# Performance work log

Hardware: AMD Instinct MI355X
Metric: run time of the kernel (lower is better)

## Reference

```python
import jax, jax.numpy as jnp
from jax import lax
import numpy as np

B, T, F = 128, 512, 64
U1_UNITS, U2_UNITS = 256, 128
W_SCALE = 0.05  # keep relu-activated cell state numerically stable


def lstm_relu(x, W, U, b, return_sequences):
    """Keras LSTM with activation='relu', recurrent_activation='sigmoid'.
    x: [B, T, D], W: [D, 4u], U: [u, 4u], b: [4u]. Gate order i, f, g, o.
    Dropout is inactive at inference and omitted."""
    Bsz = x.shape[0]
    units = U.shape[0]

    def step(carry, xt):
        h, c = carry
        z = xt @ W + h @ U + b  # [B, 4u]
        i, f, g, o = jnp.split(z, 4, axis=-1)
        i = jax.nn.sigmoid(i)
        f = jax.nn.sigmoid(f)
        g = jax.nn.relu(g)
        o = jax.nn.sigmoid(o)
        c_new = f * c + i * g
        h_new = o * jax.nn.relu(c_new)
        return (h_new, c_new), h_new

    xs = jnp.swapaxes(x, 0, 1)  # [T, B, D]
    init = (jnp.zeros((Bsz, units), x.dtype), jnp.zeros((Bsz, units), x.dtype))
    (h_last, _), hs = lax.scan(step, init, xs)
    if return_sequences:
        return jnp.swapaxes(hs, 0, 1)  # [B, T, u]
    return h_last  # [B, u]


def setup_inputs() -> dict:
    key = jax.random.key(0)
    ks = jax.random.split(key, 7)
    x = jax.random.normal(ks[0], (B, T, F), dtype=jnp.float32)
    W1 = jax.random.normal(ks[1], (F, 4 * U1_UNITS), dtype=jnp.float32) * W_SCALE
    U1 = jax.random.normal(ks[2], (U1_UNITS, 4 * U1_UNITS), dtype=jnp.float32) * W_SCALE
    b1 = jnp.zeros((4 * U1_UNITS,), dtype=jnp.float32)
    W2 = jax.random.normal(ks[3], (U1_UNITS, 4 * U2_UNITS), dtype=jnp.float32) * W_SCALE
    U2 = jax.random.normal(ks[4], (U2_UNITS, 4 * U2_UNITS), dtype=jnp.float32) * W_SCALE
    b2 = jnp.zeros((4 * U2_UNITS,), dtype=jnp.float32)
    return {"x": x, "W1": W1, "U1": U1, "b1": b1, "W2": W2, "U2": U2, "b2": b2}


def reference(x, W1, U1, b1, W2, U2, b2):
    h_seq = lstm_relu(x, W1, U1, b1, return_sequences=True)   # [B, T, 256]
    out = lstm_relu(h_seq, W2, U2, b2, return_sequences=False)  # [B, 128]
    return out
```

## Files before the change

kernel.cpp:

```cpp
#include <hip/hip_runtime.h>

#define NG 8

__device__ unsigned int g_cnt[NG * 64];

typedef __attribute__((ext_vector_type(8))) short short8;
typedef __attribute__((ext_vector_type(4))) float floatx4;

__device__ __forceinline__ unsigned int split_pack(float v) {
    unsigned int u  = __float_as_uint(v);
    unsigned int hb = u & 0xffff0000u;
    float r = v - __uint_as_float(hb);
    return hb | (__float_as_uint(r) >> 16);
}

__device__ __forceinline__ float sigmoidf_(float z) {
    return 1.0f / (1.0f + __expf(-z));
}

__device__ __forceinline__ void st_coh(unsigned int* p, unsigned int v) {
    __hip_atomic_store(p, v, __ATOMIC_RELAXED, __HIP_MEMORY_SCOPE_AGENT);
}
__device__ __forceinline__ unsigned long long ld_coh64(const unsigned long long* p) {
    return __hip_atomic_load(p, __ATOMIC_RELAXED, __HIP_MEMORY_SCOPE_AGENT);
}

template<int RS, int NJ>
__device__ __forceinline__ void stage_tile(unsigned int* lds, const unsigned int* gsrc, int tid) {
    const unsigned long long* s64 = (const unsigned long long*)gsrc;
    unsigned long long q[NJ];
#pragma unroll
    for (int j = 0; j < NJ; ++j) q[j] = ld_coh64(s64 + tid + 256 * j);
#pragma unroll
    for (int j = 0; j < NJ; ++j) {
        int f   = tid + 256 * j;
        int row = f / (RS / 2);
        int c   = (f % (RS / 2)) * 2;
        *(unsigned long long*)(lds + row * RS + (c ^ ((row & 7) << 2))) = q[j];
    }
}

__device__ __forceinline__ void unpack_lds(const unsigned int* lp, int i0, short8& ah, short8& al) {
    uint4 pa = *(const uint4*)(lp + i0);
    uint4 pb = *(const uint4*)(lp + (i0 ^ 4));
    unsigned int pv[8] = {pa.x, pa.y, pa.z, pa.w, pb.x, pb.y, pb.z, pb.w};
#pragma unroll
    for (int j = 0; j < 8; ++j) {
        ah[j] = (short)(pv[j] >> 16);
        al[j] = (short)(pv[j] & 0xffffu);
    }
}

__device__ __forceinline__ void cvt_x(const float* xp, short8& ah, short8& al) {
    float4 xa = *(const float4*)(xp);
    float4 xb = *(const float4*)(xp + 4);
    float xv[8] = {xa.x, xa.y, xa.z, xa.w, xb.x, xb.y, xb.z, xb.w};
#pragma unroll
    for (int j = 0; j < 8; ++j) {
        unsigned int u  = __float_as_uint(xv[j]);
        unsigned int hb = u & 0xffff0000u;
        float r = xv[j] - __uint_as_float(hb);
        ah[j] = (short)(u >> 16);
        al[j] = (short)(__float_as_uint(r) >> 16);
    }
}

__device__ __forceinline__ void arrive(unsigned int* cnt) {
    __hip_atomic_fetch_add(cnt, 1u, __ATOMIC_RELEASE, __HIP_MEMORY_SCOPE_AGENT);
}
__device__ __forceinline__ void spin_ge(unsigned int* cnt, unsigned int target) {
    while (__hip_atomic_fetch_add(cnt, 0u, __ATOMIC_RELAXED, __HIP_MEMORY_SCOPE_AGENT) < target) {}
}

template<int NKC, int KX, int GW, int UU, bool L1>
__device__ void lstm_role(const float* __restrict__ x,
                          const float* __restrict__ Wm, const float* __restrict__ Um,
                          const float* __restrict__ bias,
                          unsigned int* __restrict__ h1pk, unsigned int* __restrict__ h2pk,
                          float* __restrict__ out,
                          unsigned int* __restrict__ cntA, unsigned int* __restrict__ cntB,
                          int m0, int wid, float (*zex)[17],
                          unsigned int* __restrict__ ldsA, unsigned int* __restrict__ ldsB)
{
    const int tid  = threadIdx.x;
    const int lane = tid & 63;
    const int n    = lane & 15;
    const int quad = lane >> 4;
    const int gate = n >> 2;
    const int u0   = wid * 8;
    const int b_l  = lane >> 2;
    const int ul   = lane & 3;
    const int sw   = (n & 7) << 2;

    short8 bh[2][NKC], bl[2][NKC];
    float bias_v[2];
#pragma unroll
    for (int c = 0; c < 2; ++c) {
        const int col = gate * UU + u0 + c * 4 + (n & 3);
        bias_v[c] = bias[col];
#pragma unroll
        for (int kc = 0; kc < NKC; ++kc) {
#pragma unroll
            for (int j = 0; j < 8; ++j) {
                int k = kc * 32 + quad * 8 + j;
                float w = (k < KX) ? Wm[k * GW + col] : Um[(k - KX) * GW + col];
                unsigned int p = split_pack(w);
                bh[c][kc][j] = (short)(p >> 16);
                bl[c][kc][j] = (short)(p & 0xffffu);
            }
        }
    }

#pragma unroll
    for (int c = 0; c < 2; ++c) {
        if (L1) st_coh(&h1pk[32768 + (m0 + b_l) * 256 + u0 + c * 4 + ul], 0u);
        else    st_coh(&h2pk[16384 + (m0 + b_l) * 128 + u0 + c * 4 + ul], 0u);
    }
    float cst[2] = {0.f, 0.f};

    __syncthreads();
    if (tid == 0) arrive(L1 ? cntA : cntB);

    for (int s = 0; s < 512; ++s) {
        if (tid == 0) {
            if (L1) { spin_ge(cntA, 8u * (s + 1)); if (s >= 2) spin_ge(cntB, 4u * (unsigned)s); }
            else    { spin_ge(cntA, 8u * (s + 2)); spin_ge(cntB, 4u * (s + 1)); }
        }
        __syncthreads();

        if (L1) {
            stage_tile<256, 8>(ldsA, h1pk + ((s + 1) & 1) * 32768 + m0 * 256, tid);
        } else {
            stage_tile<256, 8>(ldsA, h1pk + (s & 1) * 32768 + m0 * 256, tid);
            stage_tile<128, 4>(ldsB, h2pk + ((s + 1) & 1) * 16384 + m0 * 128, tid);
        }
        __syncthreads();

        floatx4 acc[2];
#pragma unroll
        for (int c = 0; c < 2; ++c)
            acc[c] = {bias_v[c], bias_v[c], bias_v[c], bias_v[c]};

        const float* xsrc = L1 ? (x + (size_t)(m0 + n) * (512 * 64) + s * 64) : nullptr;

#pragma unroll
        for (int kc = 0; kc < NKC; ++kc) {
            short8 ah, al;
            if (L1) {
                if (kc < 2) cvt_x(xsrc + kc * 32 + quad * 8, ah, al);
                else        unpack_lds(ldsA, n * 256 + (((kc - 2) * 32 + quad * 8) ^ sw), ah, al);
            } else {
                if (kc < 8) unpack_lds(ldsA, n * 256 + ((kc * 32 + quad * 8) ^ sw), ah, al);
                else        unpack_lds(ldsB, n * 128 + (((kc - 8) * 32 + quad * 8) ^ sw), ah, al);
            }
#pragma unroll
            for (int c = 0; c < 2; ++c) {
                acc[c] = __builtin_amdgcn_mfma_f32_16x16x32_bf16(ah, bh[c][kc], acc[c], 0, 0, 0);
                acc[c] = __builtin_amdgcn_mfma_f32_16x16x32_bf16(ah, bl[c][kc], acc[c], 0, 0, 0);
                acc[c] = __builtin_amdgcn_mfma_f32_16x16x32_bf16(al, bh[c][kc], acc[c], 0, 0, 0);
            }
        }

#pragma unroll
        for (int c = 0; c < 2; ++c) {
#pragma unroll
            for (int r = 0; r < 4; ++r) zex[quad * 4 + r][n] = acc[c][r];
            asm volatile("s_waitcnt lgkmcnt(0)" ::: "memory");
            float zi = zex[b_l][ 0 + ul];
            float zf = zex[b_l][ 4 + ul];
            float zg = zex[b_l][ 8 + ul];
            float zo = zex[b_l][12 + ul];
            asm volatile("s_waitcnt lgkmcnt(0)" ::: "memory");
            float ig = sigmoidf_(zi);
            float fg = sigmoidf_(zf);
            float gg = fmaxf(zg, 0.f);
            float og = sigmoidf_(zo);
            cst[c] = fg * cst[c] + ig * gg;
            float h = og * fmaxf(cst[c], 0.f);
            unsigned int p = split_pack(h);
            int b = m0 + b_l;
            if (L1) {
                st_coh(&h1pk[(s & 1) * 32768 + b * 256 + u0 + c * 4 + ul], p);
            } else {
                st_coh(&h2pk[(s & 1) * 16384 + b * 128 + u0 + c * 4 + ul], p);
                if (s == 511) out[b * 128 + u0 + c * 4 + ul] = h;
            }
        }

        __syncthreads();
        if (tid == 0) arrive(L1 ? cntA : cntB);
    }
}

__global__ void __launch_bounds__(256, 1)
lstm_fused_kernel(const float* __restrict__ x,
                  const float* __restrict__ W1, const float* __restrict__ U1,
                  const float* __restrict__ b1,
                  const float* __restrict__ W2, const float* __restrict__ U2,
                  const float* __restrict__ b2,
                  float* __restrict__ out, unsigned int* __restrict__ ws)
{
    __shared__ float zex[4][16][17];
    __shared__ unsigned int ldsA[16 * 256];
    __shared__ unsigned int ldsB[16 * 128];
    unsigned int* h1pk = ws;
    unsigned int* h2pk = ws + 65536;
    const int g    = blockIdx.x & 7;
    const int role = blockIdx.x >> 3;
    const int wv   = threadIdx.x >> 6;
    const int m0   = g * 16;
    unsigned int* cntA = &g_cnt[g * 64];
    unsigned int* cntB = &g_cnt[g * 64 + 32];
    if (role < 8) {
        lstm_role<10, 64, 1024, 256, true >(x, W1, U1, b1, h1pk, h2pk, out,
                                            cntA, cntB, m0, role * 4 + wv, zex[wv], ldsA, ldsB);
    } else {
        lstm_role<12, 256, 512, 128, false>(x, W2, U2, b2, h1pk, h2pk, out,
                                            cntA, cntB, m0, (role - 8) * 4 + wv, zex[wv], ldsA, ldsB);
    }
}

__global__ void init_kernel(float* __restrict__ out) {
    int t = blockIdx.x * 256 + threadIdx.x;
    if (t < NG * 64) g_cnt[t] = 0u;
    if (t < 16384) out[t] = 7.0f;
}

extern "C" void kernel_launch(void* const* d_in, const int* in_sizes, int n_in,
                              void* d_out, int out_size, void* d_ws, size_t ws_size,
                              hipStream_t stream) {
    const float* x  = (const float*)d_in[0];
    const float* W1 = (const float*)d_in[1];
    const float* U1 = (const float*)d_in[2];
    const float* b1 = (const float*)d_in[3];
    const float* W2 = (const float*)d_in[4];
    const float* U2 = (const float*)d_in[5];
    const float* b2 = (const float*)d_in[6];
    float* out = (float*)d_out;
    unsigned int* ws = (unsigned int*)d_ws;
    init_kernel<<<64, 256, 0, stream>>>(out);
    lstm_fused_kernel<<<96, 256, 0, stream>>>(x, W1, U1, b1, W2, U2, b2, out, ws);
}
```

Measured before the change: 1.961 ms.

## Co-locate both LSTM layers in each block with a single skewed barrier

Each 512-thread block now holds four layer-1 waves and four layer-2 waves. Layer 2 runs one timestep behind layer 1 in a skewed loop of 513 steps. The two per-group counters become one counter with a single spin target, the grid shrinks from 96 to 64 blocks, and each block stages the h1 and h2 tiles together. The x-projection MFMAs are issued before the spin so they overlap the barrier wait. This removes a separate cross-block handshake per step, but it puts both layers behind one barrier and raises register pressure, because the merged code has 512 threads with launch bounds of 2 blocks per CU.

```diff
diff --git a/kernel.cpp b/kernel.cpp
--- a/kernel.cpp
+++ b/kernel.cpp
@@ -2,7 +2,7 @@
 
 #define NG 8
 
-__device__ unsigned int g_cnt[NG * 64];
+__device__ __attribute__((aligned(128))) unsigned int g_cnt[NG * 32];
 
 typedef __attribute__((ext_vector_type(8))) short short8;
 typedef __attribute__((ext_vector_type(4))) float floatx4;
@@ -24,19 +24,39 @@
 __device__ __forceinline__ unsigned long long ld_coh64(const unsigned long long* p) {
     return __hip_atomic_load(p, __ATOMIC_RELAXED, __HIP_MEMORY_SCOPE_AGENT);
 }
-
-template<int RS, int NJ>
-__device__ __forceinline__ void stage_tile(unsigned int* lds, const unsigned int* gsrc, int tid) {
-    const unsigned long long* s64 = (const unsigned long long*)gsrc;
-    unsigned long long q[NJ];
-#pragma unroll
-    for (int j = 0; j < NJ; ++j) q[j] = ld_coh64(s64 + tid + 256 * j);
-#pragma unroll
-    for (int j = 0; j < NJ; ++j) {
-        int f   = tid + 256 * j;
-        int row = f / (RS / 2);
-        int c   = (f % (RS / 2)) * 2;
-        *(unsigned long long*)(lds + row * RS + (c ^ ((row & 7) << 2))) = q[j];
+__device__ __forceinline__ unsigned int ld_rmw(unsigned int* p) {
+    return __hip_atomic_fetch_add(p, 0u, __ATOMIC_RELAXED, __HIP_MEMORY_SCOPE_AGENT);
+}
+__device__ __forceinline__ void arrive(unsigned int* cnt) {
+    __hip_atomic_fetch_add(cnt, 1u, __ATOMIC_RELEASE, __HIP_MEMORY_SCOPE_AGENT);
+}
+__device__ __forceinline__ void spin_ge(unsigned int* cnt, unsigned int target) {
+    while (ld_rmw(cnt) < target) {}
+}
+
+__device__ __forceinline__ void stage_both(unsigned int* ldsA, unsigned int* ldsB,
+                                           const unsigned int* srcA, const unsigned int* srcB,
+                                           int tid) {
+    const unsigned long long* sA = (const unsigned long long*)srcA;
+    const unsigned long long* sB = (const unsigned long long*)srcB;
+    unsigned long long q[6];
+#pragma unroll
+    for (int j = 0; j < 4; ++j) q[j] = ld_coh64(sA + tid + 512 * j);
+#pragma unroll
+    for (int j = 4; j < 6; ++j) q[j] = ld_coh64(sB + tid + 512 * (j - 4));
+#pragma unroll
+    for (int j = 0; j < 4; ++j) {
+        int f   = tid + 512 * j;
+        int row = f >> 7;
+        int c   = (f & 127) * 2;
+        *(unsigned long long*)(ldsA + row * 256 + (c ^ ((row & 7) << 2))) = q[j];
+    }
+#pragma unroll
+    for (int j = 4; j < 6; ++j) {
+        int f   = tid + 512 * (j - 4);
+        int row = f >> 6;
+        int c   = (f & 63) * 2;
+        *(unsigned long long*)(ldsB + row * 128 + (c ^ ((row & 7) << 2))) = q[j];
     }
 }
 
@@ -65,134 +85,7 @@
     }
 }
 
-__device__ __forceinline__ void arrive(unsigned int* cnt) {
-    __hip_atomic_fetch_add(cnt, 1u, __ATOMIC_RELEASE, __HIP_MEMORY_SCOPE_AGENT);
-}
-__device__ __forceinline__ void spin_ge(unsigned int* cnt, unsigned int target) {
-    while (__hip_atomic_fetch_add(cnt, 0u, __ATOMIC_RELAXED, __HIP_MEMORY_SCOPE_AGENT) < target) {}
-}
-
-template<int NKC, int KX, int GW, int UU, bool L1>
-__device__ void lstm_role(const float* __restrict__ x,
-                          const float* __restrict__ Wm, const float* __restrict__ Um,
-                          const float* __restrict__ bias,
-                          unsigned int* __restrict__ h1pk, unsigned int* __restrict__ h2pk,
-                          float* __restrict__ out,
-                          unsigned int* __restrict__ cntA, unsigned int* __restrict__ cntB,
-                          int m0, int wid, float (*zex)[17],
-                          unsigned int* __restrict__ ldsA, unsigned int* __restrict__ ldsB)
-{
-    const int tid  = threadIdx.x;
-    const int lane = tid & 63;
-    const int n    = lane & 15;
-    const int quad = lane >> 4;
-    const int gate = n >> 2;
-    const int u0   = wid * 8;
-    const int b_l  = lane >> 2;
-    const int ul   = lane & 3;
-    const int sw   = (n & 7) << 2;
-
-    short8 bh[2][NKC], bl[2][NKC];
-    float bias_v[2];
-#pragma unroll
-    for (int c = 0; c < 2; ++c) {
-        const int col = gate * UU + u0 + c * 4 + (n & 3);
-        bias_v[c] = bias[col];
-#pragma unroll
-        for (int kc = 0; kc < NKC; ++kc) {
-#pragma unroll
-            for (int j = 0; j < 8; ++j) {
-                int k = kc * 32 + quad * 8 + j;
-                float w = (k < KX) ? Wm[k * GW + col] : Um[(k - KX) * GW + col];
-                unsigned int p = split_pack(w);
-                bh[c][kc][j] = (short)(p >> 16);
-                bl[c][kc][j] = (short)(p & 0xffffu);
-            }
-        }
-    }
-
-#pragma unroll
-    for (int c = 0; c < 2; ++c) {
-        if (L1) st_coh(&h1pk[32768 + (m0 + b_l) * 256 + u0 + c * 4 + ul], 0u);
-        else    st_coh(&h2pk[16384 + (m0 + b_l) * 128 + u0 + c * 4 + ul], 0u);
-    }
-    float cst[2] = {0.f, 0.f};
-
-    __syncthreads();
-    if (tid == 0) arrive(L1 ? cntA : cntB);
-
-    for (int s = 0; s < 512; ++s) {
-        if (tid == 0) {
-            if (L1) { spin_ge(cntA, 8u * (s + 1)); if (s >= 2) spin_ge(cntB, 4u * (unsigned)s); }
-            else    { spin_ge(cntA, 8u * (s + 2)); spin_ge(cntB, 4u * (s + 1)); }
-        }
-        __syncthreads();
-
-        if (L1) {
-            stage_tile<256, 8>(ldsA, h1pk + ((s + 1) & 1) * 32768 + m0 * 256, tid);
-        } else {
-            stage_tile<256, 8>(ldsA, h1pk + (s & 1) * 32768 + m0 * 256, tid);
-            stage_tile<128, 4>(ldsB, h2pk + ((s + 1) & 1) * 16384 + m0 * 128, tid);
-        }
-        __syncthreads();
-
-        floatx4 acc[2];
-#pragma unroll
-        for (int c = 0; c < 2; ++c)
-            acc[c] = {bias_v[c], bias_v[c], bias_v[c], bias_v[c]};
-
-        const float* xsrc = L1 ? (x + (size_t)(m0 + n) * (512 * 64) + s * 64) : nullptr;
-
-#pragma unroll
-        for (int kc = 0; kc < NKC; ++kc) {
-            short8 ah, al;
-            if (L1) {
-                if (kc < 2) cvt_x(xsrc + kc * 32 + quad * 8, ah, al);
-                else        unpack_lds(ldsA, n * 256 + (((kc - 2) * 32 + quad * 8) ^ sw), ah, al);
-            } else {
-                if (kc < 8) unpack_lds(ldsA, n * 256 + ((kc * 32 + quad * 8) ^ sw), ah, al);
-                else        unpack_lds(ldsB, n * 128 + (((kc - 8) * 32 + quad * 8) ^ sw), ah, al);
-            }
-#pragma unroll
-            for (int c = 0; c < 2; ++c) {
-                acc[c] = __builtin_amdgcn_mfma_f32_16x16x32_bf16(ah, bh[c][kc], acc[c], 0, 0, 0);
-                acc[c] = __builtin_amdgcn_mfma_f32_16x16x32_bf16(ah, bl[c][kc], acc[c], 0, 0, 0);
-                acc[c] = __builtin_amdgcn_mfma_f32_16x16x32_bf16(al, bh[c][kc], acc[c], 0, 0, 0);
-            }
-        }
-
-#pragma unroll
-        for (int c = 0; c < 2; ++c) {
-#pragma unroll
-            for (int r = 0; r < 4; ++r) zex[quad * 4 + r][n] = acc[c][r];
-            asm volatile("s_waitcnt lgkmcnt(0)" ::: "memory");
-            float zi = zex[b_l][ 0 + ul];
-            float zf = zex[b_l][ 4 + ul];
-            float zg = zex[b_l][ 8 + ul];
-            float zo = zex[b_l][12 + ul];
-            asm volatile("s_waitcnt lgkmcnt(0)" ::: "memory");
-            float ig = sigmoidf_(zi);
-            float fg = sigmoidf_(zf);
-            float gg = fmaxf(zg, 0.f);
-            float og = sigmoidf_(zo);
-            cst[c] = fg * cst[c] + ig * gg;
-            float h = og * fmaxf(cst[c], 0.f);
-            unsigned int p = split_pack(h);
-            int b = m0 + b_l;
-            if (L1) {
-                st_coh(&h1pk[(s & 1) * 32768 + b * 256 + u0 + c * 4 + ul], p);
-            } else {
-                st_coh(&h2pk[(s & 1) * 16384 + b * 128 + u0 + c * 4 + ul], p);
-                if (s == 511) out[b * 128 + u0 + c * 4 + ul] = h;
-            }
-        }
-
-        __syncthreads();
-        if (tid == 0) arrive(L1 ? cntA : cntB);
-    }
-}
-
-__global__ void __launch_bounds__(256, 1)
+__global__ void __launch_bounds__(512, 2)
 lstm_fused_kernel(const float* __restrict__ x,
                   const float* __restrict__ W1, const float* __restrict__ U1,
                   const float* __restrict__ b1,
@@ -200,29 +93,159 @@
                   const float* __restrict__ b2,
                   float* __restrict__ out, unsigned int* __restrict__ ws)
 {
-    __shared__ float zex[4][16][17];
+    __shared__ float zex[8][16][17];
     __shared__ unsigned int ldsA[16 * 256];
     __shared__ unsigned int ldsB[16 * 128];
     unsigned int* h1pk = ws;
     unsigned int* h2pk = ws + 65536;
+
+    const int tid  = threadIdx.x;
     const int g    = blockIdx.x & 7;
-    const int role = blockIdx.x >> 3;
-    const int wv   = threadIdx.x >> 6;
+    const int blk  = blockIdx.x >> 3;
+    const int wv   = tid >> 6;
+    const bool l1w = (wv < 4);
     const int m0   = g * 16;
-    unsigned int* cntA = &g_cnt[g * 64];
-    unsigned int* cntB = &g_cnt[g * 64 + 32];
-    if (role < 8) {
-        lstm_role<10, 64, 1024, 256, true >(x, W1, U1, b1, h1pk, h2pk, out,
-                                            cntA, cntB, m0, role * 4 + wv, zex[wv], ldsA, ldsB);
-    } else {
-        lstm_role<12, 256, 512, 128, false>(x, W2, U2, b2, h1pk, h2pk, out,
-                                            cntA, cntB, m0, (role - 8) * 4 + wv, zex[wv], ldsA, ldsB);
+    unsigned int* cnt = &g_cnt[g * 32];
+
+    const int lane = tid & 63;
+    const int n    = lane & 15;
+    const int quad = lane >> 4;
+    const int gate = n >> 2;
+    const int b_l  = lane >> 2;
+    const int ul   = lane & 3;
+    const int sw   = (n & 7) << 2;
+
+    const int NKC = l1w ? 10 : 12;
+    const int NC  = l1w ? 2 : 1;
+    const int KX  = l1w ? 64 : 256;
+    const int GW  = l1w ? 1024 : 512;
+    const int UU  = l1w ? 256 : 128;
+    const int u0  = l1w ? (blk * 4 + wv) * 8
+                        : (blk * 4 + (wv - 4)) * 4;
+    const float* Wm   = l1w ? W1 : W2;
+    const float* Um   = l1w ? U1 : U2;
+    const float* bias = l1w ? b1 : b2;
+
+    short8 bh[2][12], bl[2][12];
+    float bias_v[2];
+#pragma unroll
+    for (int c = 0; c < 2; ++c) {
+        if (c >= NC) { bias_v[c] = 0.f; continue; }
+        const int col = gate * UU + u0 + c * 4 + (n & 3);
+        bias_v[c] = bias[col];
+#pragma unroll
+        for (int kc = 0; kc < 12; ++kc) {
+            if (kc >= NKC) continue;
+#pragma unroll
+            for (int j = 0; j < 8; ++j) {
+                int k = kc * 32 + quad * 8 + j;
+                float w = (k < KX) ? Wm[k * GW + col] : Um[(k - KX) * GW + col];
+                unsigned int p = split_pack(w);
+                bh[c][kc][j] = (short)(p >> 16);
+                bl[c][kc][j] = (short)(p & 0xffffu);
+            }
+        }
+    }
+
+#pragma unroll
+    for (int c = 0; c < 2; ++c) {
+        if (c >= NC) continue;
+        if (l1w) st_coh(&h1pk[32768 + (m0 + b_l) * 256 + u0 + c * 4 + ul], 0u);
+        else     st_coh(&h2pk[16384 + (m0 + b_l) * 128 + u0 + c * 4 + ul], 0u);
+    }
+    float cst[2] = {0.f, 0.f};
+
+    __syncthreads();
+    if (tid == 0) arrive(cnt);
+
+    for (int t = 0; t <= 512; ++t) {
+        floatx4 acc[2];
+#pragma unroll
+        for (int c = 0; c < 2; ++c)
+            acc[c] = {bias_v[c], bias_v[c], bias_v[c], bias_v[c]};
+        if (l1w && t < 512) {
+            const float* xsrc = x + (size_t)(m0 + n) * (512 * 64) + t * 64;
+#pragma unroll
+            for (int kc = 0; kc < 2; ++kc) {
+                short8 ah, al;
+                cvt_x(xsrc + kc * 32 + quad * 8, ah, al);
+#pragma unroll
+                for (int c = 0; c < 2; ++c) {
+                    acc[c] = __builtin_amdgcn_mfma_f32_16x16x32_bf16(ah, bh[c][kc], acc[c], 0, 0, 0);
+                    acc[c] = __builtin_amdgcn_mfma_f32_16x16x32_bf16(ah, bl[c][kc], acc[c], 0, 0, 0);
+                    acc[c] = __builtin_amdgcn_mfma_f32_16x16x32_bf16(al, bh[c][kc], acc[c], 0, 0, 0);
+                }
+            }
+        }
+
+        if (tid == 0) spin_ge(cnt, 8u * (unsigned)(t + 1));
+        __syncthreads();
+
+        stage_both(ldsA, ldsB,
+                   h1pk + ((t + 1) & 1) * 32768 + m0 * 256,
+                   h2pk + (t & 1) * 16384 + m0 * 128, tid);
+        __syncthreads();
+
+        const bool active = l1w ? (t < 512) : (t >= 1);
+        if (active) {
+            const int s = l1w ? t : (t - 1);
+
+#pragma unroll
+            for (int kc = 0; kc < 12; ++kc) {
+                if (kc >= NKC) continue;
+                if (l1w && kc < 2) continue;
+                short8 ah, al;
+                if (l1w)
+                    unpack_lds(ldsA, n * 256 + (((kc - 2) * 32 + quad * 8) ^ sw), ah, al);
+                else if (kc < 8)
+                    unpack_lds(ldsA, n * 256 + ((kc * 32 + quad * 8) ^ sw), ah, al);
+                else
+                    unpack_lds(ldsB, n * 128 + (((kc - 8) * 32 + quad * 8) ^ sw), ah, al);
+#pragma unroll
+                for (int c = 0; c < 2; ++c) {
+                    if (c >= NC) continue;
+                    acc[c] = __builtin_amdgcn_mfma_f32_16x16x32_bf16(ah, bh[c][kc], acc[c], 0, 0, 0);
+                    acc[c] = __builtin_amdgcn_mfma_f32_16x16x32_bf16(ah, bl[c][kc], acc[c], 0, 0, 0);
+                    acc[c] = __builtin_amdgcn_mfma_f32_16x16x32_bf16(al, bh[c][kc], acc[c], 0, 0, 0);
+                }
+            }
+
+#pragma unroll
+            for (int c = 0; c < 2; ++c) {
+                if (c >= NC) continue;
+#pragma unroll
+                for (int r = 0; r < 4; ++r) zex[wv][quad * 4 + r][n] = acc[c][r];
+                asm volatile("s_waitcnt lgkmcnt(0)" ::: "memory");
+                float zi = zex[wv][b_l][ 0 + ul];
+                float zf = zex[wv][b_l][ 4 + ul];
+                float zg = zex[wv][b_l][ 8 + ul];
+                float zo = zex[wv][b_l][12 + ul];
+                asm volatile("s_waitcnt lgkmcnt(0)" ::: "memory");
+                float ig = sigmoidf_(zi);
+                float fg = sigmoidf_(zf);
+                float gg = fmaxf(zg, 0.f);
+                float og = sigmoidf_(zo);
+                cst[c] = fg * cst[c] + ig * gg;
+                float h = og * fmaxf(cst[c], 0.f);
+                unsigned int p = split_pack(h);
+                int b = m0 + b_l;
+                if (l1w) {
+                    st_coh(&h1pk[(s & 1) * 32768 + b * 256 + u0 + c * 4 + ul], p);
+                } else {
+                    st_coh(&h2pk[(s & 1) * 16384 + b * 128 + u0 + c * 4 + ul], p);
+                    if (s == 511) out[b * 128 + u0 + c * 4 + ul] = h;
+                }
+            }
+        }
+
+        __syncthreads();
+        if (tid == 0 && t < 512) arrive(cnt);
     }
 }
 
 __global__ void init_kernel(float* __restrict__ out) {
     int t = blockIdx.x * 256 + threadIdx.x;
-    if (t < NG * 64) g_cnt[t] = 0u;
+    if (t < NG * 32) g_cnt[t] = 0u;
     if (t < 16384) out[t] = 7.0f;
 }
 
@@ -239,5 +262,5 @@
     float* out = (float*)d_out;
     unsigned int* ws = (unsigned int*)d_ws;
     init_kernel<<<64, 256, 0, stream>>>(out);
-    lstm_fused_kernel<<<96, 256, 0, stream>>>(x, W1, U1, b1, W2, U2, b2, out, ws);
-}
+    lstm_fused_kernel<<<64, 512, 0, stream>>>(x, W1, U1, b1, W2, U2, b2, out, ws);
+}
```

After: 2.625 ms. 1.34x slower.

## Merge LSTM worker blocks into 512-thread blocks to halve barrier participants

Applied to the files above, without the earlier changes.

Doubles the block size from 256 to 512 threads and halves the grid from 96 to 48 blocks. Each block now holds 8 waves covering twice the units, so each per-group counter barrier involves half as many arrivals (4 and 2 instead of 8 and 4), and shared-memory staging of the h tiles is split across 512 threads. The two counter spins are merged into a single polling loop. The intent is to cut cross-block synchronisation latency and redundant staging per timestep, at the cost of using fewer CUs and putting more waves on each one.

```diff
diff --git a/kernel.cpp b/kernel.cpp
--- a/kernel.cpp
+++ b/kernel.cpp
@@ -2,7 +2,7 @@
 
 #define NG 8
 
-__device__ unsigned int g_cnt[NG * 64];
+__device__ __attribute__((aligned(128))) unsigned int g_cnt[NG * 64];
 
 typedef __attribute__((ext_vector_type(8))) short short8;
 typedef __attribute__((ext_vector_type(4))) float floatx4;
@@ -24,19 +24,59 @@
 __device__ __forceinline__ unsigned long long ld_coh64(const unsigned long long* p) {
     return __hip_atomic_load(p, __ATOMIC_RELAXED, __HIP_MEMORY_SCOPE_AGENT);
 }
-
-template<int RS, int NJ>
-__device__ __forceinline__ void stage_tile(unsigned int* lds, const unsigned int* gsrc, int tid) {
+__device__ __forceinline__ unsigned int ld_rmw(unsigned int* p) {
+    return __hip_atomic_fetch_add(p, 0u, __ATOMIC_RELAXED, __HIP_MEMORY_SCOPE_AGENT);
+}
+__device__ __forceinline__ void arrive(unsigned int* cnt) {
+    __hip_atomic_fetch_add(cnt, 1u, __ATOMIC_RELEASE, __HIP_MEMORY_SCOPE_AGENT);
+}
+__device__ __forceinline__ void spin2(unsigned int* ca, unsigned int ta,
+                                      unsigned int* cb, unsigned int tb) {
+    for (;;) {
+        unsigned int ra = ld_rmw(ca);
+        unsigned int rb = ld_rmw(cb);
+        if (ra >= ta && rb >= tb) return;
+    }
+}
+
+
+__device__ __forceinline__ void stage_h1(unsigned int* lds, const unsigned int* gsrc, int tid) {
     const unsigned long long* s64 = (const unsigned long long*)gsrc;
-    unsigned long long q[NJ];
-#pragma unroll
-    for (int j = 0; j < NJ; ++j) q[j] = ld_coh64(s64 + tid + 256 * j);
-#pragma unroll
-    for (int j = 0; j < NJ; ++j) {
-        int f   = tid + 256 * j;
-        int row = f / (RS / 2);
-        int c   = (f % (RS / 2)) * 2;
-        *(unsigned long long*)(lds + row * RS + (c ^ ((row & 7) << 2))) = q[j];
+    unsigned long long q[4];
+#pragma unroll
+    for (int j = 0; j < 4; ++j) q[j] = ld_coh64(s64 + tid + 512 * j);
+#pragma unroll
+    for (int j = 0; j < 4; ++j) {
+        int f   = tid + 512 * j;
+        int row = f >> 7;
+        int c   = (f & 127) * 2;
+        *(unsigned long long*)(lds + row * 256 + (c ^ ((row & 7) << 2))) = q[j];
+    }
+}
+
+__device__ __forceinline__ void stage_h1h2(unsigned int* ldsA, unsigned int* ldsB,
+                                           const unsigned int* srcA, const unsigned int* srcB,
+                                           int tid) {
+    const unsigned long long* sA = (const unsigned long long*)srcA;
+    const unsigned long long* sB = (const unsigned long long*)srcB;
+    unsigned long long q[6];
+#pragma unroll
+    for (int j = 0; j < 4; ++j) q[j] = ld_coh64(sA + tid + 512 * j);
+#pragma unroll
+    for (int j = 4; j < 6; ++j) q[j] = ld_coh64(sB + tid + 512 * (j - 4));
+#pragma unroll
+    for (int j = 0; j < 4; ++j) {
+        int f   = tid + 512 * j;
+        int row = f >> 7;
+        int c   = (f & 127) * 2;
+        *(unsigned long long*)(ldsA + row * 256 + (c ^ ((row & 7) << 2))) = q[j];
+    }
+#pragma unroll
+    for (int j = 4; j < 6; ++j) {
+        int f   = tid + 512 * (j - 4);
+        int row = f >> 6;
+        int c   = (f & 63) * 2;
+        *(unsigned long long*)(ldsB + row * 128 + (c ^ ((row & 7) << 2))) = q[j];
     }
 }
 
@@ -63,13 +103,6 @@
         ah[j] = (short)(u >> 16);
         al[j] = (short)(__float_as_uint(r) >> 16);
     }
-}
-
-__device__ __forceinline__ void arrive(unsigned int* cnt) {
-    __hip_atomic_fetch_add(cnt, 1u, __ATOMIC_RELEASE, __HIP_MEMORY_SCOPE_AGENT);
-}
-__device__ __forceinline__ void spin_ge(unsigned int* cnt, unsigned int target) {
-    while (__hip_atomic_fetch_add(cnt, 0u, __ATOMIC_RELAXED, __HIP_MEMORY_SCOPE_AGENT) < target) {}
 }
 
 template<int NKC, int KX, int GW, int UU, bool L1>
@@ -123,16 +156,17 @@
 
     for (int s = 0; s < 512; ++s) {
         if (tid == 0) {
-            if (L1) { spin_ge(cntA, 8u * (s + 1)); if (s >= 2) spin_ge(cntB, 4u * (unsigned)s); }
-            else    { spin_ge(cntA, 8u * (s + 2)); spin_ge(cntB, 4u * (s + 1)); }
+            if (L1) spin2(cntA, 4u * (s + 1), cntB, (s >= 2) ? 2u * (unsigned)s : 0u);
+            else    spin2(cntA, 4u * (s + 2), cntB, 2u * (s + 1));
         }
         __syncthreads();
 
         if (L1) {
-            stage_tile<256, 8>(ldsA, h1pk + ((s + 1) & 1) * 32768 + m0 * 256, tid);
+            stage_h1(ldsA, h1pk + ((s + 1) & 1) * 32768 + m0 * 256, tid);
         } else {
-            stage_tile<256, 8>(ldsA, h1pk + (s & 1) * 32768 + m0 * 256, tid);
-            stage_tile<128, 4>(ldsB, h2pk + ((s + 1) & 1) * 16384 + m0 * 128, tid);
+            stage_h1h2(ldsA, ldsB,
+                       h1pk + (s & 1) * 32768 + m0 * 256,
+                       h2pk + ((s + 1) & 1) * 16384 + m0 * 128, tid);
         }
         __syncthreads();
 
@@ -192,7 +226,7 @@
     }
 }
 
-__global__ void __launch_bounds__(256, 1)
+__global__ void __launch_bounds__(512, 1)
 lstm_fused_kernel(const float* __restrict__ x,
                   const float* __restrict__ W1, const float* __restrict__ U1,
                   const float* __restrict__ b1,
@@ -200,7 +234,7 @@
                   const float* __restrict__ b2,
                   float* __restrict__ out, unsigned int* __restrict__ ws)
 {
-    __shared__ float zex[4][16][17];
+    __shared__ float zex[8][16][17];
     __shared__ unsigned int ldsA[16 * 256];
     __shared__ unsigned int ldsB[16 * 128];
     unsigned int* h1pk = ws;
@@ -211,12 +245,12 @@
     const int m0   = g * 16;
     unsigned int* cntA = &g_cnt[g * 64];
     unsigned int* cntB = &g_cnt[g * 64 + 32];
-    if (role < 8) {
+    if (role < 4) {
         lstm_role<10, 64, 1024, 256, true >(x, W1, U1, b1, h1pk, h2pk, out,
-                                            cntA, cntB, m0, role * 4 + wv, zex[wv], ldsA, ldsB);
+                                            cntA, cntB, m0, role * 8 + wv, zex[wv], ldsA, ldsB);
     } else {
         lstm_role<12, 256, 512, 128, false>(x, W2, U2, b2, h1pk, h2pk, out,
-                                            cntA, cntB, m0, (role - 8) * 4 + wv, zex[wv], ldsA, ldsB);
+                                            cntA, cntB, m0, (role - 4) * 8 + wv, zex[wv], ldsA, ldsB);
     }
 }
 
@@ -239,5 +273,5 @@
     float* out = (float*)d_out;
     unsigned int* ws = (unsigned int*)d_ws;
     init_kernel<<<64, 256, 0, stream>>>(out);
-    lstm_fused_kernel<<<96, 256, 0, stream>>>(x, W1, U1, b1, W2, U2, b2, out, ws);
-}
+    lstm_fused_kernel<<<48, 512, 0, stream>>>(x, W1, U1, b1, W2, U2, b2, out, ws);
+}
```

New measurement: 2.098 ms. +7.0%, slower.

## Load hidden state directly into registers and overlap x-projection with barrier wait

Applied to the files above, without the earlier changes.

Removes the LDS staging of the packed hidden-state tiles. Each wave now loads its own A-fragments straight from global memory with coherent 64-bit loads into registers, which drops one __syncthreads and the LDS round trip per step. In layer 1, the input-projection MFMAs on x are issued before the spin-wait, so they overlap with waiting on the other blocks. The two counter polls are also merged into one loop. The cost is redundant global loads across the four waves, since they all read the same rows, plus higher register pressure.

```diff
diff --git a/kernel.cpp b/kernel.cpp
--- a/kernel.cpp
+++ b/kernel.cpp
@@ -2,7 +2,7 @@
 
 #define NG 8
 
-__device__ unsigned int g_cnt[NG * 64];
+__device__ __attribute__((aligned(128))) unsigned int g_cnt[NG * 64];
 
 typedef __attribute__((ext_vector_type(8))) short short8;
 typedef __attribute__((ext_vector_type(4))) float floatx4;
@@ -24,30 +24,30 @@
 __device__ __forceinline__ unsigned long long ld_coh64(const unsigned long long* p) {
     return __hip_atomic_load(p, __ATOMIC_RELAXED, __HIP_MEMORY_SCOPE_AGENT);
 }
-
-template<int RS, int NJ>
-__device__ __forceinline__ void stage_tile(unsigned int* lds, const unsigned int* gsrc, int tid) {
-    const unsigned long long* s64 = (const unsigned long long*)gsrc;
-    unsigned long long q[NJ];
-#pragma unroll
-    for (int j = 0; j < NJ; ++j) q[j] = ld_coh64(s64 + tid + 256 * j);
-#pragma unroll
-    for (int j = 0; j < NJ; ++j) {
-        int f   = tid + 256 * j;
-        int row = f / (RS / 2);
-        int c   = (f % (RS / 2)) * 2;
-        *(unsigned long long*)(lds + row * RS + (c ^ ((row & 7) << 2))) = q[j];
-    }
-}
-
-__device__ __forceinline__ void unpack_lds(const unsigned int* lp, int i0, short8& ah, short8& al) {
-    uint4 pa = *(const uint4*)(lp + i0);
-    uint4 pb = *(const uint4*)(lp + (i0 ^ 4));
-    unsigned int pv[8] = {pa.x, pa.y, pa.z, pa.w, pb.x, pb.y, pb.z, pb.w};
-#pragma unroll
-    for (int j = 0; j < 8; ++j) {
-        ah[j] = (short)(pv[j] >> 16);
-        al[j] = (short)(pv[j] & 0xffffu);
+__device__ __forceinline__ unsigned int ld_rmw(unsigned int* p) {
+    return __hip_atomic_fetch_add(p, 0u, __ATOMIC_RELAXED, __HIP_MEMORY_SCOPE_AGENT);
+}
+__device__ __forceinline__ void arrive(unsigned int* cnt) {
+    __hip_atomic_fetch_add(cnt, 1u, __ATOMIC_RELEASE, __HIP_MEMORY_SCOPE_AGENT);
+}
+__device__ __forceinline__ void spin2(unsigned int* ca, unsigned int ta,
+                                      unsigned int* cb, unsigned int tb) {
+    for (;;) {
+        unsigned int ra = ld_rmw(ca);
+        unsigned int rb = ld_rmw(cb);
+        if (ra >= ta && rb >= tb) return;
+    }
+}
+
+__device__ __forceinline__ void unpack_q(const unsigned long long* q, short8& ah, short8& al) {
+#pragma unroll
+    for (int j = 0; j < 4; ++j) {
+        unsigned int lo = (unsigned int)q[j];
+        unsigned int hi = (unsigned int)(q[j] >> 32);
+        ah[2 * j]     = (short)(lo >> 16);
+        al[2 * j]     = (short)(lo & 0xffffu);
+        ah[2 * j + 1] = (short)(hi >> 16);
+        al[2 * j + 1] = (short)(hi & 0xffffu);
     }
 }
 
@@ -63,13 +63,6 @@
         ah[j] = (short)(u >> 16);
         al[j] = (short)(__float_as_uint(r) >> 16);
     }
-}
-
-__device__ __forceinline__ void arrive(unsigned int* cnt) {
-    __hip_atomic_fetch_add(cnt, 1u, __ATOMIC_RELEASE, __HIP_MEMORY_SCOPE_AGENT);
-}
-__device__ __forceinline__ void spin_ge(unsigned int* cnt, unsigned int target) {
-    while (__hip_atomic_fetch_add(cnt, 0u, __ATOMIC_RELAXED, __HIP_MEMORY_SCOPE_AGENT) < target) {}
 }
 
 template<int NKC, int KX, int GW, int UU, bool L1>
@@ -79,8 +72,7 @@
                           unsigned int* __restrict__ h1pk, unsigned int* __restrict__ h2pk,
                           float* __restrict__ out,
                           unsigned int* __restrict__ cntA, unsigned int* __restrict__ cntB,
-                          int m0, int wid, float (*zex)[17],
-                          unsigned int* __restrict__ ldsA, unsigned int* __restrict__ ldsB)
+                          int m0, int wid, float (*zex)[17])
 {
     const int tid  = threadIdx.x;
     const int lane = tid & 63;
@@ -88,9 +80,9 @@
     const int quad = lane >> 4;
     const int gate = n >> 2;
     const int u0   = wid * 8;
+    const int arow = m0 + n;
     const int b_l  = lane >> 2;
     const int ul   = lane & 3;
-    const int sw   = (n & 7) << 2;
 
     short8 bh[2][NKC], bl[2][NKC];
     float bias_v[2];
@@ -122,37 +114,60 @@
     if (tid == 0) arrive(L1 ? cntA : cntB);
 
     for (int s = 0; s < 512; ++s) {
-        if (tid == 0) {
-            if (L1) { spin_ge(cntA, 8u * (s + 1)); if (s >= 2) spin_ge(cntB, 4u * (unsigned)s); }
-            else    { spin_ge(cntA, 8u * (s + 2)); spin_ge(cntB, 4u * (s + 1)); }
-        }
-        __syncthreads();
-
-        if (L1) {
-            stage_tile<256, 8>(ldsA, h1pk + ((s + 1) & 1) * 32768 + m0 * 256, tid);
-        } else {
-            stage_tile<256, 8>(ldsA, h1pk + (s & 1) * 32768 + m0 * 256, tid);
-            stage_tile<128, 4>(ldsB, h2pk + ((s + 1) & 1) * 16384 + m0 * 128, tid);
-        }
-        __syncthreads();
-
         floatx4 acc[2];
 #pragma unroll
         for (int c = 0; c < 2; ++c)
             acc[c] = {bias_v[c], bias_v[c], bias_v[c], bias_v[c]};
-
-        const float* xsrc = L1 ? (x + (size_t)(m0 + n) * (512 * 64) + s * 64) : nullptr;
-
-#pragma unroll
-        for (int kc = 0; kc < NKC; ++kc) {
+        if (L1) {
+            const float* xsrc = x + (size_t)arow * (512 * 64) + s * 64;
+#pragma unroll
+            for (int kc = 0; kc < 2; ++kc) {
+                short8 ah, al;
+                cvt_x(xsrc + kc * 32 + quad * 8, ah, al);
+#pragma unroll
+                for (int c = 0; c < 2; ++c) {
+                    acc[c] = __builtin_amdgcn_mfma_f32_16x16x32_bf16(ah, bh[c][kc], acc[c], 0, 0, 0);
+                    acc[c] = __builtin_amdgcn_mfma_f32_16x16x32_bf16(ah, bl[c][kc], acc[c], 0, 0, 0);
+                    acc[c] = __builtin_amdgcn_mfma_f32_16x16x32_bf16(al, bh[c][kc], acc[c], 0, 0, 0);
+                }
+            }
+        }
+
+        if (tid == 0) {
+            if (L1) spin2(cntA, 8u * (s + 1), cntB, (s >= 2) ? 4u * (unsigned)s : 0u);
+            else    spin2(cntA, 8u * (s + 2), cntB, 4u * (s + 1));
+        }
+        __syncthreads();
+
+        const int NHA = L1 ? 8 : 8;
+        const unsigned long long* hA64 = (const unsigned long long*)
+            (L1 ? (h1pk + ((s + 1) & 1) * 32768 + arow * 256)
+                : (h1pk + (s & 1) * 32768 + arow * 256));
+        unsigned long long qa[8][4];
+#pragma unroll
+        for (int kc = 0; kc < 8; ++kc)
+#pragma unroll
+            for (int j = 0; j < 4; ++j)
+                qa[kc][j] = ld_coh64(hA64 + kc * 16 + quad * 4 + j);
+
+        unsigned long long qb[4][4];
+        if (!L1) {
+            const unsigned long long* hB64 = (const unsigned long long*)
+                (h2pk + ((s + 1) & 1) * 16384 + arow * 128);
+#pragma unroll
+            for (int kc = 0; kc < 4; ++kc)
+#pragma unroll
+                for (int j = 0; j < 4; ++j)
+                    qb[kc][j] = ld_coh64(hB64 + kc * 16 + quad * 4 + j);
+        }
+        (void)NHA;
+
+#pragma unroll
+        for (int kc = (L1 ? 2 : 0); kc < NKC; ++kc) {
             short8 ah, al;
-            if (L1) {
-                if (kc < 2) cvt_x(xsrc + kc * 32 + quad * 8, ah, al);
-                else        unpack_lds(ldsA, n * 256 + (((kc - 2) * 32 + quad * 8) ^ sw), ah, al);
-            } else {
-                if (kc < 8) unpack_lds(ldsA, n * 256 + ((kc * 32 + quad * 8) ^ sw), ah, al);
-                else        unpack_lds(ldsB, n * 128 + (((kc - 8) * 32 + quad * 8) ^ sw), ah, al);
-            }
+            if (L1)           unpack_q(qa[kc - 2], ah, al);
+            else if (kc < 8)  unpack_q(qa[kc], ah, al);
+            else              unpack_q(qb[kc - 8], ah, al);
 #pragma unroll
             for (int c = 0; c < 2; ++c) {
                 acc[c] = __builtin_amdgcn_mfma_f32_16x16x32_bf16(ah, bh[c][kc], acc[c], 0, 0, 0);
@@ -201,8 +216,6 @@
                   float* __restrict__ out, unsigned int* __restrict__ ws)
 {
     __shared__ float zex[4][16][17];
-    __shared__ unsigned int ldsA[16 * 256];
-    __shared__ unsigned int ldsB[16 * 128];
     unsigned int* h1pk = ws;
     unsigned int* h2pk = ws + 65536;
     const int g    = blockIdx.x & 7;
@@ -213,10 +226,10 @@
     unsigned int* cntB = &g_cnt[g * 64 + 32];
     if (role < 8) {
         lstm_role<10, 64, 1024, 256, true >(x, W1, U1, b1, h1pk, h2pk, out,
-                                            cntA, cntB, m0, role * 4 + wv, zex[wv], ldsA, ldsB);
+                                            cntA, cntB, m0, role * 4 + wv, zex[wv]);
     } else {
         lstm_role<12, 256, 512, 128, false>(x, W2, U2, b2, h1pk, h2pk, out,
-                                            cntA, cntB, m0, (role - 8) * 4 + wv, zex[wv], ldsA, ldsB);
+                                            cntA, cntB, m0, (role - 8) * 4 + wv, zex[wv]);
     }
 }
 
```

After: 3.749 ms. 91.2% more time.
